# Optimization experiments

Hardware: AMD Instinct MI355X
Metric: run time of the kernel (lower is better)

Reference implementation:

```python
import jax, jax.numpy as jnp
import numpy as np

B, C, T, HEADS = 4, 1024, 1024, 16


def setup_inputs() -> dict:
    key = jax.random.key(0)
    k0, k1, k2, k3 = jax.random.split(key, 4)
    x = jax.random.normal(k0, (B, C, T), dtype=jnp.float32)
    mask = jax.random.randint(k1, (B, T), 0, 2).astype(bool)  # True = masked position
    scale = 1.0 / np.sqrt(C).astype(np.float32)
    w_kvq = jax.random.normal(k2, (3 * C, C), dtype=jnp.float32) * scale  # Conv1d k=1, no bias
    w_out = jax.random.normal(k3, (C, C), dtype=jnp.float32) * scale
    return {"x": x, "mask": mask, "w_kvq": w_kvq, "w_out": w_out}


def reference(x, mask, w_kvq, w_out):
    b, c, t = x.shape
    h = HEADS
    d = c // h  # head dim; torch scales by sqrt(k.size(1)) = sqrt(d)
    # Conv1d with kernel 1 == per-timestep matmul over channels
    kvq = jnp.einsum('oc,bct->bot', w_kvq, x)  # [B, 3C, T]
    k, v, q = jnp.split(kvq, 3, axis=1)        # each [B, C, T]
    k = k.reshape(b, h, d, t)
    v = v.reshape(b, h, d, t)
    q = q.reshape(b, h, d, t)
    # att[b,h,i,j] = <k_i, q_j> / sqrt(d); i = key pos, j = query pos
    att = jnp.einsum('bhdi,bhdj->bhij', k, q) / jnp.sqrt(jnp.asarray(d, x.dtype))
    # pre-softmax: mask key positions (dim i) with -inf
    att = jnp.where(mask[:, None, :, None], -jnp.inf, att)
    att = jax.nn.softmax(att, axis=2)  # softmax over keys (torch dim=1 of [Bh,Tk,Tq])
    # post-softmax: zero out masked query positions (dim j)
    att = jnp.where(mask[:, None, None, :], jnp.asarray(0.0, x.dtype), att)
    o = jnp.einsum('bhdi,bhij->bhdj', v, att)  # [B, h, d, T]
    o = o.reshape(b, c, t)
    out = x + jnp.einsum('oc,bct->bot', w_out, o)
    # match torch layout: cat over heads along batch dim -> [h*B, T, T]
    att_flat = jnp.transpose(att, (1, 0, 2, 3)).reshape(h * b, t, t)
    return out, att_flat
```

## Files before the change

### kernel.cpp

```cpp
#include <hip/hip_runtime.h>

#define BB 4
#define CC 1024
#define TT 1024
#define HH 16
#define DD 64

typedef __bf16 v8bf __attribute__((ext_vector_type(8)));
typedef __bf16 v4bf __attribute__((ext_vector_type(4)));
typedef float  v4f  __attribute__((ext_vector_type(4)));

__global__ __launch_bounds__(256) void expand_mask_kernel(const void* mraw, float* maskf) {
  __shared__ int flagA, flagB;
  if (threadIdx.x == 0) { flagA = 0; flagB = 0; }
  __syncthreads();
  const unsigned char* mb = (const unsigned char*)mraw;
  const int n = BB * TT;
  int a = 0, bfl = 0;
  for (int i = threadIdx.x; i < n; i += 256) {
    if (mb[i]) { if ((i & 3) == 0) a = 1; else bfl = 1; }
  }
  if (a)   atomicOr(&flagA, 1);
  if (bfl) atomicOr(&flagB, 1);
  __syncthreads();
  int layout;
  if (flagA && !flagB)      layout = 0;
  else if (!flagA && flagB) layout = 1;
  else                      layout = 2;
  for (int i = threadIdx.x; i < n; i += 256) {
    float m;
    if (layout == 0)      m = (((const int*)mraw)[i]   != 0)   ? 1.f : 0.f;
    else if (layout == 1) m = (((const float*)mraw)[i] != 0.f) ? 1.f : 0.f;
    else                  m = (mb[i] != 0)                     ? 1.f : 0.f;
    maskf[i] = m;
  }
}

__global__ __launch_bounds__(256) void cast_f32_bf16(const float* __restrict__ src,
                                                     __bf16* __restrict__ dst, int n) {
  int i = (blockIdx.x * 256 + threadIdx.x) * 8;
  if (i >= n) return;
  float4 f0 = *(const float4*)(src + i);
  float4 f1 = *(const float4*)(src + i + 4);
  v8bf o;
  o[0] = (__bf16)f0.x; o[1] = (__bf16)f0.y; o[2] = (__bf16)f0.z; o[3] = (__bf16)f0.w;
  o[4] = (__bf16)f1.x; o[5] = (__bf16)f1.y; o[6] = (__bf16)f1.z; o[7] = (__bf16)f1.w;
  *(v8bf*)(dst + i) = o;
}

__global__ __launch_bounds__(256) void transpose_x(const float* __restrict__ x,
                                                   __bf16* __restrict__ xT) {
  const int b = blockIdx.z;
  const int t0 = blockIdx.x * 64, c0 = blockIdx.y * 64;
  __shared__ __bf16 T[64][72];
  const int tid = threadIdx.x;
  {
    int row = tid >> 2, coff = (tid & 3) * 16;
    const float* src = x + ((long)b * CC + c0 + row) * TT + t0 + coff;
#pragma unroll
    for (int s = 0; s < 4; s++) {
      float4 f = *(const float4*)(src + s * 4);
      T[row][coff + s * 4 + 0] = (__bf16)f.x;
      T[row][coff + s * 4 + 1] = (__bf16)f.y;
      T[row][coff + s * 4 + 2] = (__bf16)f.z;
      T[row][coff + s * 4 + 3] = (__bf16)f.w;
    }
  }
  __syncthreads();
  {
    int trow = tid >> 2, ccoff = (tid & 3) * 16;
    __bf16 vals[16];
#pragma unroll
    for (int i = 0; i < 16; i++) vals[i] = T[ccoff + i][trow];
    __bf16* dst = xT + ((long)b * TT + t0 + trow) * CC + c0 + ccoff;
    *(v8bf*)dst       = *(v8bf*)&vals[0];
    *(v8bf*)(dst + 8) = *(v8bf*)&vals[8];
  }
}

__global__ __launch_bounds__(256) void transpose_kq(const __bf16* __restrict__ kvqb,
                                                    __bf16* __restrict__ kqT) {
  const int zz = blockIdx.z;
  const int b = zz >> 1, part = zz & 1;
  const int srcbase = part == 0 ? 0 : 2 * CC;
  const int dstbase = part * CC;
  const int t0 = blockIdx.x * 64, c0 = blockIdx.y * 64;
  __shared__ __bf16 T[64][72];
  const int tid = threadIdx.x;
  {
    int row = tid >> 2, coff = (tid & 3) * 16;
    const __bf16* src = kvqb + ((long)b * 3 * CC + srcbase + c0 + row) * TT + t0 + coff;
    *(v8bf*)&T[row][coff]     = *(const v8bf*)src;
    *(v8bf*)&T[row][coff + 8] = *(const v8bf*)(src + 8);
  }
  __syncthreads();
  {
    int trow = tid >> 2, ccoff = (tid & 3) * 16;
    __bf16 vals[16];
#pragma unroll
    for (int i = 0; i < 16; i++) vals[i] = T[ccoff + i][trow];
    __bf16* dst = kqT + ((long)b * TT + t0 + trow) * (2 * CC) + dstbase + c0 + ccoff;
    *(v8bf*)dst       = *(v8bf*)&vals[0];
    *(v8bf*)(dst + 8) = *(v8bf*)&vals[8];
  }
}

template <int MODE>
__global__ __launch_bounds__(256) void gemm_bt(
    const __bf16* __restrict__ A, const __bf16* __restrict__ BTfull,
    const float* __restrict__ Sfull, void* __restrict__ Ofull,
    long strideBT, long strideOS)
{
  const __bf16* BT = BTfull + (long)blockIdx.z * strideBT;
  const int m0 = blockIdx.y * 128, n0 = blockIdx.x * 128;
  __shared__ __bf16 As[128][48];
  __shared__ __bf16 Bs[128][48];
  const int tid = threadIdx.x;
  const int lane = tid & 63, wave = tid >> 6;
  const int wm = wave >> 1, wn = wave & 1;
  const int ln = lane & 15, q = lane >> 4;

  v4f acc[4][4];
#pragma unroll
  for (int i = 0; i < 4; i++)
#pragma unroll
    for (int j = 0; j < 4; j++) acc[i][j] = (v4f)(0.f);

  const int srow = tid >> 2, skc = (tid & 3) * 8;
  for (int k0 = 0; k0 < CC; k0 += 32) {
#pragma unroll
    for (int s = 0; s < 2; s++) {
      int row = srow + s * 64;
      *(v8bf*)&As[row][skc] = *(const v8bf*)(A  + (long)(m0 + row) * CC + k0 + skc);
      *(v8bf*)&Bs[row][skc] = *(const v8bf*)(BT + (long)(n0 + row) * CC + k0 + skc);
    }
    __syncthreads();
    v8bf af[4], bf[4];
#pragma unroll
    for (int mi = 0; mi < 4; mi++) af[mi] = *(v8bf*)&As[wm * 64 + mi * 16 + ln][q * 8];
#pragma unroll
    for (int ni = 0; ni < 4; ni++) bf[ni] = *(v8bf*)&Bs[wn * 64 + ni * 16 + ln][q * 8];
#pragma unroll
    for (int mi = 0; mi < 4; mi++)
#pragma unroll
      for (int ni = 0; ni < 4; ni++)
        acc[mi][ni] = __builtin_amdgcn_mfma_f32_16x16x32_bf16(af[mi], bf[ni], acc[mi][ni], 0, 0, 0);
    __syncthreads();
  }
#pragma unroll
  for (int mi = 0; mi < 4; mi++)
#pragma unroll
    for (int ni = 0; ni < 4; ni++)
#pragma unroll
      for (int r = 0; r < 4; r++) {
        int row = m0 + wm * 64 + mi * 16 + q * 4 + r;
        int col = n0 + wn * 64 + ni * 16 + ln;
        if (MODE == 0) {
          ((__bf16*)Ofull)[(long)blockIdx.z * strideOS + (long)row * TT + col] = (__bf16)acc[mi][ni][r];
        } else {
          long off = (long)blockIdx.z * strideOS + (long)row * TT + col;
          ((float*)Ofull)[off] = acc[mi][ni][r] + Sfull[off];
        }
      }
}

__global__ __launch_bounds__(256) void attn_stats(
    const __bf16* __restrict__ kqT, const float* __restrict__ maskf,
    float* __restrict__ pmax, float* __restrict__ psum)
{
  const int z = blockIdx.z, h = z >> 2, b = z & 3;
  const int i0 = blockIdx.y * 128, j0 = blockIdx.x * 128;
  __shared__ __bf16 Ks[128][72];
  __shared__ __bf16 Qs[128][72];
  const __bf16* kbase = kqT + (long)b * TT * (2 * CC);
  const int tid = threadIdx.x;
#pragma unroll
  for (int s = 0; s < 4; s++) {
    int c = tid + s * 256;
    int row = c >> 3, off = (c & 7) * 8;
    *(v8bf*)&Ks[row][off] = *(const v8bf*)(kbase + (long)(i0 + row) * (2 * CC) + h * DD + off);
    *(v8bf*)&Qs[row][off] = *(const v8bf*)(kbase + (long)(j0 + row) * (2 * CC) + CC + h * DD + off);
  }
  __syncthreads();
  const int lane = tid & 63, wave = tid >> 6;
  const int wi = wave >> 1, wj = wave & 1;
  const int ln = lane & 15, q = lane >> 4;

  v8bf ak[4][2], bq[4][2];
#pragma unroll
  for (int mi = 0; mi < 4; mi++)
#pragma unroll
    for (int kd = 0; kd < 2; kd++)
      ak[mi][kd] = *(v8bf*)&Ks[wi * 64 + mi * 16 + ln][kd * 32 + q * 8];
#pragma unroll
  for (int ni = 0; ni < 4; ni++)
#pragma unroll
    for (int kd = 0; kd < 2; kd++)
      bq[ni][kd] = *(v8bf*)&Qs[wj * 64 + ni * 16 + ln][kd * 32 + q * 8];

  v4f acc[4][4];
#pragma unroll
  for (int mi = 0; mi < 4; mi++)
#pragma unroll
    for (int ni = 0; ni < 4; ni++) {
      v4f a = (v4f)(0.f);
      a = __builtin_amdgcn_mfma_f32_16x16x32_bf16(ak[mi][0], bq[ni][0], a, 0, 0, 0);
      a = __builtin_amdgcn_mfma_f32_16x16x32_bf16(ak[mi][1], bq[ni][1], a, 0, 0, 0);
      acc[mi][ni] = a;
    }

  float kmv[4][4];
#pragma unroll
  for (int mi = 0; mi < 4; mi++)
#pragma unroll
    for (int r = 0; r < 4; r++)
      kmv[mi][r] = maskf[b * TT + i0 + wi * 64 + mi * 16 + q * 4 + r];

#pragma unroll
  for (int ni = 0; ni < 4; ni++) {
    float lv[16];
    float m = -3.4e38f;
#pragma unroll
    for (int mi = 0; mi < 4; mi++)
#pragma unroll
      for (int r = 0; r < 4; r++) {
        float l = (kmv[mi][r] != 0.f) ? -1e30f : acc[mi][ni][r] * 0.125f;
        lv[mi * 4 + r] = l;
        m = fmaxf(m, l);
      }
    float s = 0.f;
#pragma unroll
    for (int i = 0; i < 16; i++) s += __expf(lv[i] - m);
#pragma unroll
    for (int off = 16; off <= 32; off <<= 1) {
      float om = __shfl_xor(m, off, 64);
      float os = __shfl_xor(s, off, 64);
      float M = fmaxf(m, om);
      s = s * __expf(m - M) + os * __expf(om - M);
      m = M;
    }
    if (q == 0) {
      long so = ((long)z * 16 + (i0 >> 6) + wi) * TT + j0 + wj * 64 + ni * 16 + ln;
      pmax[so] = m;
      psum[so] = s;
    }
  }
}

__global__ __launch_bounds__(256) void combine_stats(
    const float* __restrict__ pmax, const float* __restrict__ psum,
    const float* __restrict__ maskf, float2* __restrict__ fstats)
{
  const int z = blockIdx.y;
  const int b = z & 3;
  const int j = blockIdx.x * 256 + threadIdx.x;
  float M = -3.4e38f;
  float pm[16];
#pragma unroll
  for (int t = 0; t < 16; t++) {
    pm[t] = pmax[((long)z * 16 + t) * TT + j];
    M = fmaxf(M, pm[t]);
  }
  float S = 0.f;
#pragma unroll
  for (int t = 0; t < 16; t++)
    S += psum[((long)z * 16 + t) * TT + j] * __expf(pm[t] - M);
  const float qz = (maskf[b * TT + j] != 0.f) ? 0.f : 1.f;
  fstats[(long)z * TT + j] = make_float2(M, qz / S);
}

__global__ __launch_bounds__(256) void gemm_pv(
    const __bf16* __restrict__ kqT, const __bf16* __restrict__ kvqb,
    const float2* __restrict__ fstats, const float* __restrict__ maskf,
    float* __restrict__ att, __bf16* __restrict__ oT)
{
  const int z = blockIdx.y, h = z >> 2, b = z & 3;
  const int j0 = blockIdx.x * 64;
  __shared__ __align__(16) char smem[50176];
  __bf16 (*Qs)[72] = (__bf16(*)[72])smem;
  float* km = (float*)(smem + 9216 + 4 * 9216);
  const int tid = threadIdx.x;
  const int lane = tid & 63, wave = tid >> 6;
  const int ln = lane & 15, q = lane >> 4;
  __bf16 (*Pt)[72] = (__bf16(*)[72])(smem + 9216 + wave * 9216);

  const __bf16* kbase = kqT + (long)b * TT * (2 * CC);
  const __bf16* vbase = kvqb + (long)(b * 3 * CC + CC + h * DD) * TT;

#pragma unroll
  for (int s = 0; s < 2; s++) {
    int c = tid + s * 256;
    int row = c >> 3, off = (c & 7) * 8;
    *(v8bf*)&Qs[row][off] = *(const v8bf*)(kbase + (long)(j0 + row) * (2 * CC) + CC + h * DD + off);
  }
  {
    float4 f = *(const float4*)(maskf + b * TT + tid * 4);
    *(float4*)&km[tid * 4] = f;
  }
  __syncthreads();

  v8bf bq[4][2];
#pragma unroll
  for (int ni = 0; ni < 4; ni++)
#pragma unroll
    for (int kd = 0; kd < 2; kd++)
      bq[ni][kd] = *(v8bf*)&Qs[ni * 16 + ln][kd * 32 + q * 8];
  float2 st[4];
#pragma unroll
  for (int ni = 0; ni < 4; ni++) st[ni] = fstats[(long)z * TT + j0 + ni * 16 + ln];

  v4f acc[4][4];
#pragma unroll
  for (int i = 0; i < 4; i++)
#pragma unroll
    for (int j = 0; j < 4; j++) acc[i][j] = (v4f)(0.f);

  for (int it = 0; it < 4; it++) {
    const int ibase = wave * 256 + it * 64;
#pragma unroll
    for (int mi = 0; mi < 4; mi++) {
      const __bf16* arow = kbase + (long)(ibase + mi * 16 + ln) * (2 * CC) + h * DD;
      v8bf ak0 = *(const v8bf*)(arow + q * 8);
      v8bf ak1 = *(const v8bf*)(arow + 32 + q * 8);
#pragma unroll
      for (int ni = 0; ni < 4; ni++) {
        v4f l4 = (v4f)(0.f);
        l4 = __builtin_amdgcn_mfma_f32_16x16x32_bf16(ak0, bq[ni][0], l4, 0, 0, 0);
        l4 = __builtin_amdgcn_mfma_f32_16x16x32_bf16(ak1, bq[ni][1], l4, 0, 0, 0);
        v4bf pb;
#pragma unroll
        for (int r = 0; r < 4; r++) {
          int i_loc = mi * 16 + q * 4 + r;
          int i_glob = ibase + i_loc;
          float l = (km[i_glob] != 0.f) ? -1e30f : l4[r] * 0.125f;
          float p = __expf(l - st[ni].x) * st[ni].y;
          att[((long)z << 20) + (long)i_glob * TT + j0 + ni * 16 + ln] = p;
          pb[r] = (__bf16)p;
        }
        *(v4bf*)&Pt[ni * 16 + ln][mi * 16 + q * 4] = pb;
      }
    }
    v8bf ap[4][2], bv[4][2];
#pragma unroll
    for (int ji = 0; ji < 4; ji++)
#pragma unroll
      for (int ki = 0; ki < 2; ki++)
        ap[ji][ki] = *(v8bf*)&Pt[ji * 16 + ln][ki * 32 + q * 8];
#pragma unroll
    for (int di = 0; di < 4; di++)
#pragma unroll
      for (int ki = 0; ki < 2; ki++)
        bv[di][ki] = *(const v8bf*)(vbase + (long)(di * 16 + ln) * TT + ibase + ki * 32 + q * 8);
#pragma unroll
    for (int ji = 0; ji < 4; ji++)
#pragma unroll
      for (int di = 0; di < 4; di++) {
        acc[ji][di] = __builtin_amdgcn_mfma_f32_16x16x32_bf16(ap[ji][0], bv[di][0], acc[ji][di], 0, 0, 0);
        acc[ji][di] = __builtin_amdgcn_mfma_f32_16x16x32_bf16(ap[ji][1], bv[di][1], acc[ji][di], 0, 0, 0);
      }
  }

  float (*red)[68] = (float(*)[68])(smem + 9216);
  for (int w = 0; w < 4; w++) {
    __syncthreads();
    if (wave == w) {
#pragma unroll
      for (int ji = 0; ji < 4; ji++)
#pragma unroll
        for (int di = 0; di < 4; di++)
#pragma unroll
          for (int r = 0; r < 4; r++) {
            int row = ji * 16 + q * 4 + r;
            int col = di * 16 + ln;
            if (w == 0) red[row][col] = acc[ji][di][r];
            else        red[row][col] += acc[ji][di][r];
          }
    }
  }
  __syncthreads();
  {
    int row = tid >> 2, c0 = (tid & 3) * 16;
    __bf16 ob[16];
#pragma unroll
    for (int i = 0; i < 16; i++) ob[i] = (__bf16)red[row][c0 + i];
    __bf16* dst = oT + ((long)b * TT + j0 + row) * CC + h * DD + c0;
    *(v8bf*)dst       = *(v8bf*)&ob[0];
    *(v8bf*)(dst + 8) = *(v8bf*)&ob[8];
  }
}

extern "C" void kernel_launch(void* const* d_in, const int* in_sizes, int n_in,
                              void* d_out, int out_size, void* d_ws, size_t ws_size,
                              hipStream_t stream) {
  const float* x     = (const float*)d_in[0];
  const void*  mask  = d_in[1];
  const float* w_kvq = (const float*)d_in[2];
  const float* w_out = (const float*)d_in[3];

  float* out = (float*)d_out;
  float* att = out + (long)BB * CC * TT;

  char* wsb = (char*)d_ws;
  float*   maskf = (float*)(wsb + 0);
  __bf16*  wkb   = (__bf16*)(wsb + 16384);
  __bf16*  wob   = (__bf16*)(wsb + 6307840);
  __bf16*  xT    = (__bf16*)(wsb + 8404992);
  __bf16*  kqT   = (__bf16*)(wsb + 8404992);
  __bf16*  kvqb  = (__bf16*)(wsb + 25182208);
  __bf16*  oT    = (__bf16*)(wsb + 50348032);
  float*   pmax  = (float*)(wsb + 58736640);
  float*   psum  = (float*)(wsb + 62930944);
  float2*  fst   = (float2*)(wsb + 67125248);

  expand_mask_kernel<<<1, 256, 0, stream>>>(mask, maskf);
  cast_f32_bf16<<<(3 * CC * CC) / 2048, 256, 0, stream>>>(w_kvq, wkb, 3 * CC * CC);
  cast_f32_bf16<<<(CC * CC) / 2048, 256, 0, stream>>>(w_out, wob, CC * CC);
  transpose_x<<<dim3(16, 16, BB), 256, 0, stream>>>(x, xT);
  gemm_bt<0><<<dim3(8, 24, BB), 256, 0, stream>>>(
      wkb, xT, nullptr, kvqb, (long)CC * TT, (long)3 * CC * TT);
  transpose_kq<<<dim3(16, 16, 2 * BB), 256, 0, stream>>>(kvqb, kqT);
  attn_stats<<<dim3(8, 8, HH * BB), 256, 0, stream>>>(kqT, maskf, pmax, psum);
  combine_stats<<<dim3(4, HH * BB), 256, 0, stream>>>(pmax, psum, maskf, fst);
  gemm_pv<<<dim3(16, HH * BB), 256, 0, stream>>>(kqT, kvqb, fst, maskf, att, oT);
  gemm_bt<1><<<dim3(8, 8, BB), 256, 0, stream>>>(
      wob, oT, x, out, (long)CC * TT, (long)CC * TT);
}
```

Measured before the change: 467.9 us.

## Fuse prep kernels, transposed QKV epilogue, online softmax stats, global_load_lds GEMM staging

Merges mask expansion and both weight casts into one prep launch. The QKV GEMM epilogue now writes K and Q transposed through LDS and V separately, which removes the transpose_kq kernel. The two-pass attention stats plus combine are replaced by a single kernel that streams all keys with an online max/sum and reduces across waves in LDS. GEMM tile staging now uses global_load_lds direct-to-LDS loads without padding, which may add bank conflicts on the fragment reads.

```diff
diff --git a/kernel.cpp b/kernel.cpp
--- a/kernel.cpp
+++ b/kernel.cpp
@@ -10,42 +10,54 @@
 typedef __bf16 v4bf __attribute__((ext_vector_type(4)));
 typedef float  v4f  __attribute__((ext_vector_type(4)));
 
-__global__ __launch_bounds__(256) void expand_mask_kernel(const void* mraw, float* maskf) {
-  __shared__ int flagA, flagB;
-  if (threadIdx.x == 0) { flagA = 0; flagB = 0; }
-  __syncthreads();
-  const unsigned char* mb = (const unsigned char*)mraw;
-  const int n = BB * TT;
-  int a = 0, bfl = 0;
-  for (int i = threadIdx.x; i < n; i += 256) {
-    if (mb[i]) { if ((i & 3) == 0) a = 1; else bfl = 1; }
-  }
-  if (a)   atomicOr(&flagA, 1);
-  if (bfl) atomicOr(&flagB, 1);
-  __syncthreads();
-  int layout;
-  if (flagA && !flagB)      layout = 0;
-  else if (!flagA && flagB) layout = 1;
-  else                      layout = 2;
-  for (int i = threadIdx.x; i < n; i += 256) {
-    float m;
-    if (layout == 0)      m = (((const int*)mraw)[i]   != 0)   ? 1.f : 0.f;
-    else if (layout == 1) m = (((const float*)mraw)[i] != 0.f) ? 1.f : 0.f;
-    else                  m = (mb[i] != 0)                     ? 1.f : 0.f;
-    maskf[i] = m;
-  }
-}
-
-__global__ __launch_bounds__(256) void cast_f32_bf16(const float* __restrict__ src,
-                                                     __bf16* __restrict__ dst, int n) {
-  int i = (blockIdx.x * 256 + threadIdx.x) * 8;
-  if (i >= n) return;
-  float4 f0 = *(const float4*)(src + i);
-  float4 f1 = *(const float4*)(src + i + 4);
+__device__ __forceinline__ void gl_lds16(const __bf16* g, __bf16* l) {
+  __builtin_amdgcn_global_load_lds(
+      (const __attribute__((address_space(1))) void*)g,
+      (__attribute__((address_space(3))) void*)l, 16, 0, 0);
+}
+
+__global__ __launch_bounds__(256) void prep(
+    const void* mraw, float* __restrict__ maskf,
+    const float* __restrict__ w_kvq, const float* __restrict__ w_out,
+    __bf16* __restrict__ wkb, __bf16* __restrict__ wob)
+{
+  if (blockIdx.x == 0) {
+    __shared__ int flagA, flagB;
+    if (threadIdx.x == 0) { flagA = 0; flagB = 0; }
+    __syncthreads();
+    const unsigned char* mb = (const unsigned char*)mraw;
+    const int n = BB * TT;
+    int a = 0, bfl = 0;
+    for (int i = threadIdx.x; i < n; i += 256) {
+      if (mb[i]) { if ((i & 3) == 0) a = 1; else bfl = 1; }
+    }
+    if (a)   atomicOr(&flagA, 1);
+    if (bfl) atomicOr(&flagB, 1);
+    __syncthreads();
+    int layout;
+    if (flagA && !flagB)      layout = 0;
+    else if (!flagA && flagB) layout = 1;
+    else                      layout = 2;
+    for (int i = threadIdx.x; i < n; i += 256) {
+      float m;
+      if (layout == 0)      m = (((const int*)mraw)[i]   != 0)   ? 1.f : 0.f;
+      else if (layout == 1) m = (((const float*)mraw)[i] != 0.f) ? 1.f : 0.f;
+      else                  m = (mb[i] != 0)                     ? 1.f : 0.f;
+      maskf[i] = m;
+    }
+    return;
+  }
+  long i = ((long)blockIdx.x - 1) * 2048 + threadIdx.x * 8;
+  const float* src;
+  __bf16* dst;
+  if (i < (long)3 * CC * CC) { src = w_kvq + i; dst = wkb + i; }
+  else { long j = i - (long)3 * CC * CC; src = w_out + j; dst = wob + j; }
+  float4 f0 = *(const float4*)src;
+  float4 f1 = *(const float4*)(src + 4);
   v8bf o;
   o[0] = (__bf16)f0.x; o[1] = (__bf16)f0.y; o[2] = (__bf16)f0.z; o[3] = (__bf16)f0.w;
   o[4] = (__bf16)f1.x; o[5] = (__bf16)f1.y; o[6] = (__bf16)f1.z; o[7] = (__bf16)f1.w;
-  *(v8bf*)(dst + i) = o;
+  *(v8bf*)dst = o;
 }
 
 __global__ __launch_bounds__(256) void transpose_x(const float* __restrict__ x,
@@ -78,43 +90,19 @@
   }
 }
 
-__global__ __launch_bounds__(256) void transpose_kq(const __bf16* __restrict__ kvqb,
-                                                    __bf16* __restrict__ kqT) {
-  const int zz = blockIdx.z;
-  const int b = zz >> 1, part = zz & 1;
-  const int srcbase = part == 0 ? 0 : 2 * CC;
-  const int dstbase = part * CC;
-  const int t0 = blockIdx.x * 64, c0 = blockIdx.y * 64;
-  __shared__ __bf16 T[64][72];
-  const int tid = threadIdx.x;
-  {
-    int row = tid >> 2, coff = (tid & 3) * 16;
-    const __bf16* src = kvqb + ((long)b * 3 * CC + srcbase + c0 + row) * TT + t0 + coff;
-    *(v8bf*)&T[row][coff]     = *(const v8bf*)src;
-    *(v8bf*)&T[row][coff + 8] = *(const v8bf*)(src + 8);
-  }
-  __syncthreads();
-  {
-    int trow = tid >> 2, ccoff = (tid & 3) * 16;
-    __bf16 vals[16];
-#pragma unroll
-    for (int i = 0; i < 16; i++) vals[i] = T[ccoff + i][trow];
-    __bf16* dst = kqT + ((long)b * TT + t0 + trow) * (2 * CC) + dstbase + c0 + ccoff;
-    *(v8bf*)dst       = *(v8bf*)&vals[0];
-    *(v8bf*)(dst + 8) = *(v8bf*)&vals[8];
-  }
-}
-
 template <int MODE>
 __global__ __launch_bounds__(256) void gemm_bt(
     const __bf16* __restrict__ A, const __bf16* __restrict__ BTfull,
-    const float* __restrict__ Sfull, void* __restrict__ Ofull,
-    long strideBT, long strideOS)
+    const float* __restrict__ Sfull, float* __restrict__ Ofull,
+    __bf16* __restrict__ kqT, __bf16* __restrict__ vbuf,
+    long strideBT)
 {
-  const __bf16* BT = BTfull + (long)blockIdx.z * strideBT;
+  const int bz = blockIdx.z;
+  const __bf16* BT = BTfull + (long)bz * strideBT;
   const int m0 = blockIdx.y * 128, n0 = blockIdx.x * 128;
-  __shared__ __bf16 As[128][48];
-  __shared__ __bf16 Bs[128][48];
+  __shared__ __align__(16) char smem[(MODE == 0) ? 34816 : 16384];
+  __bf16 (*As)[32] = (__bf16(*)[32])smem;
+  __bf16 (*Bs)[32] = (__bf16(*)[32])(smem + 8192);
   const int tid = threadIdx.x;
   const int lane = tid & 63, wave = tid >> 6;
   const int wm = wave >> 1, wn = wave & 1;
@@ -126,13 +114,14 @@
 #pragma unroll
     for (int j = 0; j < 4; j++) acc[i][j] = (v4f)(0.f);
 
-  const int srow = tid >> 2, skc = (tid & 3) * 8;
+  const int lr = lane >> 2;
+  const int lc = (lane & 3) * 8;
   for (int k0 = 0; k0 < CC; k0 += 32) {
 #pragma unroll
     for (int s = 0; s < 2; s++) {
-      int row = srow + s * 64;
-      *(v8bf*)&As[row][skc] = *(const v8bf*)(A  + (long)(m0 + row) * CC + k0 + skc);
-      *(v8bf*)&Bs[row][skc] = *(const v8bf*)(BT + (long)(n0 + row) * CC + k0 + skc);
+      int row = wave * 32 + s * 16;
+      gl_lds16(A  + (long)(m0 + row + lr) * CC + k0 + lc, &As[row][0]);
+      gl_lds16(BT + (long)(n0 + row + lr) * CC + k0 + lc, &Bs[row][0]);
     }
     __syncthreads();
     v8bf af[4], bf[4];
@@ -147,90 +136,118 @@
         acc[mi][ni] = __builtin_amdgcn_mfma_f32_16x16x32_bf16(af[mi], bf[ni], acc[mi][ni], 0, 0, 0);
     __syncthreads();
   }
-#pragma unroll
-  for (int mi = 0; mi < 4; mi++)
-#pragma unroll
-    for (int ni = 0; ni < 4; ni++)
-#pragma unroll
-      for (int r = 0; r < 4; r++) {
-        int row = m0 + wm * 64 + mi * 16 + q * 4 + r;
-        int col = n0 + wn * 64 + ni * 16 + ln;
-        if (MODE == 0) {
-          ((__bf16*)Ofull)[(long)blockIdx.z * strideOS + (long)row * TT + col] = (__bf16)acc[mi][ni][r];
-        } else {
-          long off = (long)blockIdx.z * strideOS + (long)row * TT + col;
-          ((float*)Ofull)[off] = acc[mi][ni][r] + Sfull[off];
+
+  if (MODE == 1) {
+#pragma unroll
+    for (int mi = 0; mi < 4; mi++)
+#pragma unroll
+      for (int ni = 0; ni < 4; ni++)
+#pragma unroll
+        for (int r = 0; r < 4; r++) {
+          long off = (long)bz * CC * TT + (long)(m0 + wm * 64 + mi * 16 + q * 4 + r) * TT
+                   + n0 + wn * 64 + ni * 16 + ln;
+          Ofull[off] = acc[mi][ni][r] + Sfull[off];
+        }
+  } else {
+    const int third = m0 >> 10;
+    if (third == 1) {
+      const int mb = m0 - 1024;
+#pragma unroll
+      for (int mi = 0; mi < 4; mi++)
+#pragma unroll
+        for (int ni = 0; ni < 4; ni++)
+#pragma unroll
+          for (int r = 0; r < 4; r++)
+            vbuf[((long)bz * CC + mb + wm * 64 + mi * 16 + q * 4 + r) * TT
+                 + n0 + wn * 64 + ni * 16 + ln] = (__bf16)acc[mi][ni][r];
+    } else {
+      __bf16 (*Tl)[136] = (__bf16(*)[136])smem;
+#pragma unroll
+      for (int mi = 0; mi < 4; mi++)
+#pragma unroll
+        for (int ni = 0; ni < 4; ni++) {
+          v4bf pb;
+#pragma unroll
+          for (int r = 0; r < 4; r++) pb[r] = (__bf16)acc[mi][ni][r];
+          *(v4bf*)&Tl[wn * 64 + ni * 16 + ln][wm * 64 + mi * 16 + q * 4] = pb;
+        }
+      __syncthreads();
+      const int dstbase = (third == 0) ? 0 : CC;
+      const int mcol = (third == 0) ? m0 : (m0 - 2048);
+      int t = tid >> 1, c0 = (tid & 1) * 64;
+      __bf16* drow = kqT + ((long)bz * TT + n0 + t) * (2 * CC) + dstbase + mcol + c0;
+#pragma unroll
+      for (int s = 0; s < 8; s++)
+        *(v8bf*)(drow + s * 8) = *(v8bf*)&Tl[t][c0 + s * 8];
+    }
+  }
+}
+
+__global__ __launch_bounds__(256) void attn_fstats(
+    const __bf16* __restrict__ kqT, const float* __restrict__ maskf,
+    float2* __restrict__ fstats)
+{
+  const int z = blockIdx.y, h = z >> 2, b = z & 3;
+  const int j0 = blockIdx.x * 64;
+  const __bf16* kbase = kqT + (long)b * TT * (2 * CC);
+  const int tid = threadIdx.x;
+  const int lane = tid & 63, wave = tid >> 6;
+  const int ln = lane & 15, q = lane >> 4;
+  __shared__ float2 red[4][64];
+
+  v8bf bq[4][2];
+#pragma unroll
+  for (int ni = 0; ni < 4; ni++)
+#pragma unroll
+    for (int kd = 0; kd < 2; kd++)
+      bq[ni][kd] = *(const v8bf*)(kbase + (long)(j0 + ni * 16 + ln) * (2 * CC)
+                                  + CC + h * DD + kd * 32 + q * 8);
+
+  float rm[4], rs[4];
+#pragma unroll
+  for (int ni = 0; ni < 4; ni++) { rm[ni] = -3.4e38f; rs[ni] = 0.f; }
+
+  for (int it = 0; it < 4; it++) {
+    const int ibase = wave * 256 + it * 64;
+    float4 km4[4];
+    v8bf ak[4][2];
+#pragma unroll
+    for (int mi = 0; mi < 4; mi++) {
+      km4[mi] = *(const float4*)(maskf + b * TT + ibase + mi * 16 + q * 4);
+#pragma unroll
+      for (int kd = 0; kd < 2; kd++)
+        ak[mi][kd] = *(const v8bf*)(kbase + (long)(ibase + mi * 16 + ln) * (2 * CC)
+                                    + h * DD + kd * 32 + q * 8);
+    }
+#pragma unroll
+    for (int ni = 0; ni < 4; ni++) {
+      float lv[16];
+      float cm = -3.4e38f;
+#pragma unroll
+      for (int mi = 0; mi < 4; mi++) {
+        v4f l4 = (v4f)(0.f);
+        l4 = __builtin_amdgcn_mfma_f32_16x16x32_bf16(ak[mi][0], bq[ni][0], l4, 0, 0, 0);
+        l4 = __builtin_amdgcn_mfma_f32_16x16x32_bf16(ak[mi][1], bq[ni][1], l4, 0, 0, 0);
+#pragma unroll
+        for (int r = 0; r < 4; r++) {
+          float km = (r == 0) ? km4[mi].x : (r == 1) ? km4[mi].y : (r == 2) ? km4[mi].z : km4[mi].w;
+          float l = (km != 0.f) ? -1e30f : l4[r] * 0.125f;
+          lv[mi * 4 + r] = l;
+          cm = fmaxf(cm, l);
         }
       }
-}
-
-__global__ __launch_bounds__(256) void attn_stats(
-    const __bf16* __restrict__ kqT, const float* __restrict__ maskf,
-    float* __restrict__ pmax, float* __restrict__ psum)
-{
-  const int z = blockIdx.z, h = z >> 2, b = z & 3;
-  const int i0 = blockIdx.y * 128, j0 = blockIdx.x * 128;
-  __shared__ __bf16 Ks[128][72];
-  __shared__ __bf16 Qs[128][72];
-  const __bf16* kbase = kqT + (long)b * TT * (2 * CC);
-  const int tid = threadIdx.x;
-#pragma unroll
-  for (int s = 0; s < 4; s++) {
-    int c = tid + s * 256;
-    int row = c >> 3, off = (c & 7) * 8;
-    *(v8bf*)&Ks[row][off] = *(const v8bf*)(kbase + (long)(i0 + row) * (2 * CC) + h * DD + off);
-    *(v8bf*)&Qs[row][off] = *(const v8bf*)(kbase + (long)(j0 + row) * (2 * CC) + CC + h * DD + off);
-  }
-  __syncthreads();
-  const int lane = tid & 63, wave = tid >> 6;
-  const int wi = wave >> 1, wj = wave & 1;
-  const int ln = lane & 15, q = lane >> 4;
-
-  v8bf ak[4][2], bq[4][2];
-#pragma unroll
-  for (int mi = 0; mi < 4; mi++)
-#pragma unroll
-    for (int kd = 0; kd < 2; kd++)
-      ak[mi][kd] = *(v8bf*)&Ks[wi * 64 + mi * 16 + ln][kd * 32 + q * 8];
-#pragma unroll
-  for (int ni = 0; ni < 4; ni++)
-#pragma unroll
-    for (int kd = 0; kd < 2; kd++)
-      bq[ni][kd] = *(v8bf*)&Qs[wj * 64 + ni * 16 + ln][kd * 32 + q * 8];
-
-  v4f acc[4][4];
-#pragma unroll
-  for (int mi = 0; mi < 4; mi++)
-#pragma unroll
-    for (int ni = 0; ni < 4; ni++) {
-      v4f a = (v4f)(0.f);
-      a = __builtin_amdgcn_mfma_f32_16x16x32_bf16(ak[mi][0], bq[ni][0], a, 0, 0, 0);
-      a = __builtin_amdgcn_mfma_f32_16x16x32_bf16(ak[mi][1], bq[ni][1], a, 0, 0, 0);
-      acc[mi][ni] = a;
-    }
-
-  float kmv[4][4];
-#pragma unroll
-  for (int mi = 0; mi < 4; mi++)
-#pragma unroll
-    for (int r = 0; r < 4; r++)
-      kmv[mi][r] = maskf[b * TT + i0 + wi * 64 + mi * 16 + q * 4 + r];
+      float nm = fmaxf(rm[ni], cm);
+      float s = 0.f;
+#pragma unroll
+      for (int i = 0; i < 16; i++) s += __expf(lv[i] - nm);
+      rs[ni] = rs[ni] * __expf(rm[ni] - nm) + s;
+      rm[ni] = nm;
+    }
+  }
 
 #pragma unroll
   for (int ni = 0; ni < 4; ni++) {
-    float lv[16];
-    float m = -3.4e38f;
-#pragma unroll
-    for (int mi = 0; mi < 4; mi++)
-#pragma unroll
-      for (int r = 0; r < 4; r++) {
-        float l = (kmv[mi][r] != 0.f) ? -1e30f : acc[mi][ni][r] * 0.125f;
-        lv[mi * 4 + r] = l;
-        m = fmaxf(m, l);
-      }
-    float s = 0.f;
-#pragma unroll
-    for (int i = 0; i < 16; i++) s += __expf(lv[i] - m);
+    float m = rm[ni], s = rs[ni];
 #pragma unroll
     for (int off = 16; off <= 32; off <<= 1) {
       float om = __shfl_xor(m, off, 64);
@@ -239,38 +256,24 @@
       s = s * __expf(m - M) + os * __expf(om - M);
       m = M;
     }
-    if (q == 0) {
-      long so = ((long)z * 16 + (i0 >> 6) + wi) * TT + j0 + wj * 64 + ni * 16 + ln;
-      pmax[so] = m;
-      psum[so] = s;
-    }
-  }
-}
-
-__global__ __launch_bounds__(256) void combine_stats(
-    const float* __restrict__ pmax, const float* __restrict__ psum,
-    const float* __restrict__ maskf, float2* __restrict__ fstats)
-{
-  const int z = blockIdx.y;
-  const int b = z & 3;
-  const int j = blockIdx.x * 256 + threadIdx.x;
-  float M = -3.4e38f;
-  float pm[16];
-#pragma unroll
-  for (int t = 0; t < 16; t++) {
-    pm[t] = pmax[((long)z * 16 + t) * TT + j];
-    M = fmaxf(M, pm[t]);
-  }
-  float S = 0.f;
-#pragma unroll
-  for (int t = 0; t < 16; t++)
-    S += psum[((long)z * 16 + t) * TT + j] * __expf(pm[t] - M);
-  const float qz = (maskf[b * TT + j] != 0.f) ? 0.f : 1.f;
-  fstats[(long)z * TT + j] = make_float2(M, qz / S);
+    if (q == 0) red[wave][ni * 16 + ln] = make_float2(m, s);
+  }
+  __syncthreads();
+  if (tid < 64) {
+    float M = -3.4e38f;
+    float2 v[4];
+#pragma unroll
+    for (int w = 0; w < 4; w++) { v[w] = red[w][tid]; M = fmaxf(M, v[w].x); }
+    float S = 0.f;
+#pragma unroll
+    for (int w = 0; w < 4; w++) S += v[w].y * __expf(v[w].x - M);
+    const float qz = (maskf[b * TT + j0 + tid] != 0.f) ? 0.f : 1.f;
+    fstats[(long)z * TT + j0 + tid] = make_float2(M, qz / S);
+  }
 }
 
 __global__ __launch_bounds__(256) void gemm_pv(
-    const __bf16* __restrict__ kqT, const __bf16* __restrict__ kvqb,
+    const __bf16* __restrict__ kqT, const __bf16* __restrict__ vbuf,
     const float2* __restrict__ fstats, const float* __restrict__ maskf,
     float* __restrict__ att, __bf16* __restrict__ oT)
 {
@@ -285,7 +288,7 @@
   __bf16 (*Pt)[72] = (__bf16(*)[72])(smem + 9216 + wave * 9216);
 
   const __bf16* kbase = kqT + (long)b * TT * (2 * CC);
-  const __bf16* vbase = kvqb + (long)(b * 3 * CC + CC + h * DD) * TT;
+  const __bf16* vbase = vbuf + ((long)b * CC + h * DD) * TT;
 
 #pragma unroll
   for (int s = 0; s < 2; s++) {
@@ -405,23 +408,17 @@
   __bf16*  wkb   = (__bf16*)(wsb + 16384);
   __bf16*  wob   = (__bf16*)(wsb + 6307840);
   __bf16*  xT    = (__bf16*)(wsb + 8404992);
-  __bf16*  kqT   = (__bf16*)(wsb + 8404992);
-  __bf16*  kvqb  = (__bf16*)(wsb + 25182208);
-  __bf16*  oT    = (__bf16*)(wsb + 50348032);
-  float*   pmax  = (float*)(wsb + 58736640);
-  float*   psum  = (float*)(wsb + 62930944);
-  float2*  fst   = (float2*)(wsb + 67125248);
-
-  expand_mask_kernel<<<1, 256, 0, stream>>>(mask, maskf);
-  cast_f32_bf16<<<(3 * CC * CC) / 2048, 256, 0, stream>>>(w_kvq, wkb, 3 * CC * CC);
-  cast_f32_bf16<<<(CC * CC) / 2048, 256, 0, stream>>>(w_out, wob, CC * CC);
+  __bf16*  kqT   = (__bf16*)(wsb + 16793600);
+  __bf16*  vbuf  = (__bf16*)(wsb + 33570816);
+  __bf16*  oT    = (__bf16*)(wsb + 41959424);
+  float2*  fst   = (float2*)(wsb + 50348032);
+
+  prep<<<2049, 256, 0, stream>>>(mask, maskf, w_kvq, w_out, wkb, wob);
   transpose_x<<<dim3(16, 16, BB), 256, 0, stream>>>(x, xT);
   gemm_bt<0><<<dim3(8, 24, BB), 256, 0, stream>>>(
-      wkb, xT, nullptr, kvqb, (long)CC * TT, (long)3 * CC * TT);
-  transpose_kq<<<dim3(16, 16, 2 * BB), 256, 0, stream>>>(kvqb, kqT);
-  attn_stats<<<dim3(8, 8, HH * BB), 256, 0, stream>>>(kqT, maskf, pmax, psum);
-  combine_stats<<<dim3(4, HH * BB), 256, 0, stream>>>(pmax, psum, maskf, fst);
-  gemm_pv<<<dim3(16, HH * BB), 256, 0, stream>>>(kqT, kvqb, fst, maskf, att, oT);
+      wkb, xT, nullptr, nullptr, kqT, vbuf, (long)CC * TT);
+  attn_fstats<<<dim3(16, HH * BB), 256, 0, stream>>>(kqT, maskf, fst);
+  gemm_pv<<<dim3(16, HH * BB), 256, 0, stream>>>(kqT, vbuf, fst, maskf, att, oT);
   gemm_bt<1><<<dim3(8, 8, BB), 256, 0, stream>>>(
-      wob, oT, x, out, (long)CC * TT, (long)CC * TT);
-}
+      wob, oT, x, out, nullptr, nullptr, (long)CC * TT);
+}
```

Measured after the change: 471.2 us. About the same (+0.7%).
